# Performance work log

Hardware: AMD Instinct MI355X
Metric: run time of the kernel (lower is better)

Reference implementation:

```python
import jax, jax.numpy as jnp
import numpy as np

B, S, D, EXP = 2, 2048, 128, 16
N = D * EXP  # state_dim = 2048


def setup_inputs() -> dict:
    key = jax.random.key(0)
    ks = jax.random.split(key, 11)
    s_in = 1.0 / np.sqrt(D)   # torch Linear default init bound for dim->N layers
    s_out = 1.0 / np.sqrt(N)  # for out_proj (N->dim)
    x = jax.random.normal(ks[0], (B, S, D), dtype=jnp.float32)
    W_B = jax.random.uniform(ks[1], (N, D), jnp.float32, -s_in, s_in)
    b_B = jax.random.uniform(ks[2], (N,), jnp.float32, -s_in, s_in)
    W_C = jax.random.uniform(ks[3], (N, D), jnp.float32, -s_in, s_in)
    b_C = jax.random.uniform(ks[4], (N,), jnp.float32, -s_in, s_in)
    W_dt = jax.random.uniform(ks[5], (N, D), jnp.float32, -s_in, s_in)
    b_dt = jax.random.uniform(ks[6], (N,), jnp.float32, -s_in, s_in)
    A_log = jnp.log(jax.random.uniform(ks[7], (N,), jnp.float32) * 0.5 + 0.5)
    W_out = jax.random.uniform(ks[8], (D, N), jnp.float32, -s_out, s_out)
    b_out = jax.random.uniform(ks[9], (D,), jnp.float32, -s_out, s_out)
    return {"x": x, "W_B": W_B, "b_B": b_B, "W_C": W_C, "b_C": b_C,
            "W_dt": W_dt, "b_dt": b_dt, "A_log": A_log,
            "W_out": W_out, "b_out": b_out}


def reference(x, W_B, b_B, W_C, b_C, W_dt, b_dt, A_log, W_out, b_out):
    # Featurizer projections: [B,S,D] -> [B,S,N]
    B_feat = jnp.einsum('bsd,nd->bsn', x, W_B) + b_B
    C_feat = jnp.einsum('bsd,nd->bsn', x, W_C) + b_C
    dt = jax.nn.softplus(jnp.einsum('bsd,nd->bsn', x, W_dt) + b_dt)
    A = -jnp.exp(A_log)                # [N]
    A_bar = jnp.exp(dt * A)            # [B,S,N]
    B_bar = dt * B_feat                # [B,S,N]

    # Sequential diagonal scan: h_t = A_t * h_{t-1} + B_t ; y_t = C_t * h_t
    def step(h, abc):
        a_t, b_t, c_t = abc            # each [B,N]
        h = a_t * h + b_t
        return h, c_t * h

    h0 = jnp.zeros((x.shape[0], N), dtype=x.dtype)
    xs = (jnp.swapaxes(A_bar, 0, 1),   # [S,B,N]
          jnp.swapaxes(B_bar, 0, 1),
          jnp.swapaxes(C_feat, 0, 1))
    _, ys = jax.lax.scan(step, h0, xs)  # ys: [S,B,N]
    y = jnp.swapaxes(ys, 0, 1)          # [B,S,N]
    return jnp.einsum('bsn,dn->bsd', y, W_out) + b_out
```

## Files before the change

kernel.cpp:

```cpp
#include <hip/hip_runtime.h>


#define BB 2
#define SS 2048
#define DDIM 128
#define NDIM 2048
#define TT (BB*SS)
#define NTILE (TT/16)
#define TPB 128

typedef short short8 __attribute__((ext_vector_type(8)));
typedef float floatx4 __attribute__((ext_vector_type(4)));

__device__ __forceinline__ unsigned short f2b(float f){
  unsigned u = __float_as_uint(f);
  u += 0x7FFFu + ((u >> 16) & 1u);
  return (unsigned short)(u >> 16);
}
__device__ __forceinline__ float softplus_f(float v){
  return v > 15.f ? v : __logf(1.f + __expf(v));
}
__device__ __forceinline__ void pack8(const float* __restrict__ s,
                                      unsigned short* __restrict__ d){
  floatx4 v0 = *(const floatx4*)s;
  floatx4 v1 = *(const floatx4*)(s + 4);
  short8 r;
  r[0]=(short)f2b(v0[0]); r[1]=(short)f2b(v0[1]); r[2]=(short)f2b(v0[2]); r[3]=(short)f2b(v0[3]);
  r[4]=(short)f2b(v1[0]); r[5]=(short)f2b(v1[1]); r[6]=(short)f2b(v1[2]); r[7]=(short)f2b(v1[3]);
  *(short8*)d = r;
}

__global__ void prep_kernel(const float* __restrict__ x,
                            const float* __restrict__ W_B,
                            const float* __restrict__ W_C,
                            const float* __restrict__ W_dt,
                            const float* __restrict__ A_log,
                            const float* __restrict__ W_out,
                            unsigned short* __restrict__ xp,
                            unsigned short* __restrict__ Wp3,
                            unsigned short* __restrict__ Wop,
                            float* __restrict__ Aval){
  const int gid = blockIdx.x * blockDim.x + threadIdx.x;
  if (gid < 2048) Aval[gid] = -__expf(A_log[gid]);
  if (gid < 65536){
    int g = gid, tile = g >> 8, kk = (g >> 6) & 3, lane = g & 63;
    int q = lane >> 4, m = lane & 15;
    pack8(x + (size_t)(tile*16 + m)*DDIM + kk*32 + q*8, xp + (size_t)g*8);
  }
  if (gid < 98304){
    int mat = gid >> 15, g = gid & 32767;
    const float* W = (mat == 0) ? W_B : (mat == 1 ? W_dt : W_C);
    int tile = g >> 8, kk = (g >> 6) & 3, lane = g & 63;
    int q = lane >> 4, m = lane & 15;
    pack8(W + (size_t)(tile*16 + m)*DDIM + kk*32 + q*8,
          Wp3 + (size_t)mat*262144 + (size_t)g*8);
  }
  if (gid < 32768){
    int g = gid, tile = g >> 12, kk = (g >> 6) & 63, lane = g & 63;
    int q = lane >> 4, m = lane & 15;
    pack8(W_out + (size_t)(tile*16 + m)*NDIM + kk*32 + q*8, Wop + (size_t)g*8);
  }
}

__global__ void projscan1_kernel(const unsigned short* __restrict__ xp,
                                 const unsigned short* __restrict__ Wp3,
                                 const float* __restrict__ b_B,
                                 const float* __restrict__ b_dt,
                                 const float* __restrict__ Aval,
                                 float2* __restrict__ PH){
  __shared__ unsigned short sW[2*8192];
  const int tid  = threadIdx.x;
  const int lane = tid & 63;
  const int wv   = tid >> 6;
  const int m    = lane & 15;
  const int q    = lane >> 4;

#pragma unroll
  for (int mat = 0; mat < 2; ++mat){
    const unsigned short* src = Wp3 + (size_t)mat*262144 + (size_t)blockIdx.y*8192;
    unsigned short* dst = sW + mat*8192;
#pragma unroll
    for (int i = 0; i < 4; ++i){
      int e = (i*256 + tid) * 8;
      *(short8*)(dst + e) = *(const short8*)(src + e);
    }
  }
  __syncthreads();

  const int tileT = blockIdx.x*4 + wv;
  short8 xf[4];
#pragma unroll
  for (int kk = 0; kk < 4; ++kk)
    xf[kk] = *(const short8*)(xp + (size_t)tileT*2048 + kk*512 + lane*8);

  floatx4 acc[2][4];
#pragma unroll
  for (int mat = 0; mat < 2; ++mat)
#pragma unroll
    for (int nt = 0; nt < 4; ++nt)
      acc[mat][nt] = (floatx4){0.f,0.f,0.f,0.f};
#pragma unroll
  for (int nt = 0; nt < 4; ++nt)
#pragma unroll
    for (int kk = 0; kk < 4; ++kk){
      short8 wB = *(const short8*)(sW +          nt*2048 + kk*512 + lane*8);
      short8 wD = *(const short8*)(sW + 8192 +   nt*2048 + kk*512 + lane*8);
      acc[0][nt] = __builtin_amdgcn_mfma_f32_16x16x32_bf16(xf[kk], wB, acc[0][nt], 0, 0, 0);
      acc[1][nt] = __builtin_amdgcn_mfma_f32_16x16x32_bf16(xf[kk], wD, acc[1][nt], 0, 0, 0);
    }

  const int n0 = blockIdx.y*64;
#pragma unroll
  for (int nt = 0; nt < 4; ++nt){
    const int n = n0 + nt*16 + m;
    const float bB = b_B[n], bD = b_dt[n], Av = Aval[n];
    float Ar[4], Br[4];
#pragma unroll
    for (int r = 0; r < 4; ++r){
      float dtv = softplus_f(acc[1][nt][r] + bD);
      Ar[r] = __expf(dtv * Av);
      Br[r] = dtv * (acc[0][nt][r] + bB);
    }
    float P = Ar[0], H = Br[0];
#pragma unroll
    for (int r = 1; r < 4; ++r){ H = Ar[r]*H + Br[r]; P *= Ar[r]; }
    float pp = __shfl(P, (lane - 16) & 63, 64);
    float hh = __shfl(H, (lane - 16) & 63, 64);
    if (q >= 1){ H = P*hh + H; P = P*pp; }
    pp = __shfl(P, (lane - 32) & 63, 64);
    hh = __shfl(H, (lane - 32) & 63, 64);
    if (q >= 2){ H = P*hh + H; P = P*pp; }
    if (q == 3){
      float2 ph; ph.x = P; ph.y = H;
      PH[(size_t)tileT*NDIM + n] = ph;
    }
  }
}

__global__ void carry_kernel(const float2* __restrict__ PH,
                             float* __restrict__ initb){
  __shared__ float sP[8][32], sH[8][32], eP[8][32], eH[8][32];
  const int tid = threadIdx.x;
  const int c = tid & 31;
  const int s = tid >> 5;
  const int b = blockIdx.x >> 6;
  const int n = (blockIdx.x & 63)*32 + c;

  float Pj[16], Hj[16];
  size_t base = ((size_t)(b*TPB + s*16))*NDIM + n;
#pragma unroll
  for (int j = 0; j < 16; ++j){
    float2 ph = PH[base + (size_t)j*NDIM];
    Pj[j] = ph.x; Hj[j] = ph.y;
  }
  float P = Pj[0], H = Hj[0];
#pragma unroll
  for (int j = 1; j < 16; ++j){ H = Pj[j]*H + Hj[j]; P *= Pj[j]; }
  sP[s][c] = P; sH[s][c] = H;
  __syncthreads();
  if (tid < 32){
    float p = 1.f, h = 0.f;
#pragma unroll
    for (int ss = 0; ss < 8; ++ss){
      eP[ss][tid] = p; eH[ss][tid] = h;
      h = sP[ss][tid]*h + sH[ss][tid];
      p = sP[ss][tid]*p;
    }
  }
  __syncthreads();
  float h = eH[s][c];
#pragma unroll
  for (int j = 0; j < 16; ++j){
    initb[base + (size_t)j*NDIM] = h;
    h = Pj[j]*h + Hj[j];
  }
}

__global__ void projscan2_kernel(const unsigned short* __restrict__ xp,
                                 const unsigned short* __restrict__ Wp3,
                                 const float* __restrict__ b_B,
                                 const float* __restrict__ b_dt,
                                 const float* __restrict__ b_C,
                                 const float* __restrict__ Aval,
                                 const float* __restrict__ initb,
                                 unsigned short* __restrict__ ybp){
  __shared__ unsigned short sW[3*8192];
  __shared__ unsigned short sYT[4][16*40];
  const int tid  = threadIdx.x;
  const int lane = tid & 63;
  const int wv   = tid >> 6;
  const int m    = lane & 15;
  const int q    = lane >> 4;

#pragma unroll
  for (int mat = 0; mat < 3; ++mat){
    const unsigned short* src = Wp3 + (size_t)mat*262144 + (size_t)blockIdx.y*8192;
    unsigned short* dst = sW + mat*8192;
#pragma unroll
    for (int i = 0; i < 4; ++i){
      int e = (i*256 + tid) * 8;
      *(short8*)(dst + e) = *(const short8*)(src + e);
    }
  }
  __syncthreads();

  const int tileT = blockIdx.x*4 + wv;
  short8 xf[4];
#pragma unroll
  for (int kk = 0; kk < 4; ++kk)
    xf[kk] = *(const short8*)(xp + (size_t)tileT*2048 + kk*512 + lane*8);

  floatx4 acc[3][4];
#pragma unroll
  for (int mat = 0; mat < 3; ++mat)
#pragma unroll
    for (int nt = 0; nt < 4; ++nt)
      acc[mat][nt] = (floatx4){0.f,0.f,0.f,0.f};
#pragma unroll
  for (int nt = 0; nt < 4; ++nt)
#pragma unroll
    for (int kk = 0; kk < 4; ++kk){
      short8 wB = *(const short8*)(sW +           nt*2048 + kk*512 + lane*8);
      short8 wD = *(const short8*)(sW + 8192 +    nt*2048 + kk*512 + lane*8);
      short8 wC = *(const short8*)(sW + 16384 +   nt*2048 + kk*512 + lane*8);
      acc[0][nt] = __builtin_amdgcn_mfma_f32_16x16x32_bf16(xf[kk], wB, acc[0][nt], 0, 0, 0);
      acc[1][nt] = __builtin_amdgcn_mfma_f32_16x16x32_bf16(xf[kk], wD, acc[1][nt], 0, 0, 0);
      acc[2][nt] = __builtin_amdgcn_mfma_f32_16x16x32_bf16(xf[kk], wC, acc[2][nt], 0, 0, 0);
    }

  const int n0 = blockIdx.y*64;
  unsigned short ybuf[16];
#pragma unroll
  for (int nt = 0; nt < 4; ++nt){
    const int n = n0 + nt*16 + m;
    const float bB = b_B[n], bD = b_dt[n], bC = b_C[n], Av = Aval[n];
    const float iv = initb[(size_t)tileT*NDIM + n];
    float Ar[4], Br[4], Cc[4];
#pragma unroll
    for (int r = 0; r < 4; ++r){
      float dtv = softplus_f(acc[1][nt][r] + bD);
      Ar[r] = __expf(dtv * Av);
      Br[r] = dtv * (acc[0][nt][r] + bB);
      Cc[r] = acc[2][nt][r] + bC;
    }
    float P = Ar[0], H = Br[0];
#pragma unroll
    for (int r = 1; r < 4; ++r){ H = Ar[r]*H + Br[r]; P *= Ar[r]; }
    float pp = __shfl(P, (lane - 16) & 63, 64);
    float hh = __shfl(H, (lane - 16) & 63, 64);
    if (q >= 1){ H = P*hh + H; P = P*pp; }
    pp = __shfl(P, (lane - 32) & 63, 64);
    hh = __shfl(H, (lane - 32) & 63, 64);
    if (q >= 2){ H = P*hh + H; P = P*pp; }
    float pe = __shfl(P, (lane - 16) & 63, 64);
    float he = __shfl(H, (lane - 16) & 63, 64);
    if (q == 0){ pe = 1.f; he = 0.f; }
    float h = pe*iv + he;
#pragma unroll
    for (int r = 0; r < 4; ++r){
      h = Ar[r]*h + Br[r];
      ybuf[nt*4 + r] = f2b(Cc[r]*h);
    }
  }
#pragma unroll
  for (int p = 0; p < 2; ++p){
#pragma unroll
    for (int nt2 = 0; nt2 < 2; ++nt2){
      const int nt = 2*p + nt2;
#pragma unroll
      for (int r = 0; r < 4; ++r)
        sYT[wv][(q*4 + r)*40 + nt2*16 + m] = ybuf[nt*4 + r];
    }
    short8 af = *(const short8*)&sYT[wv][m*40 + q*8];
    const int kchunk = blockIdx.y*2 + p;
    *(short8*)(ybp + (size_t)tileT*32768 + (size_t)kchunk*512 + lane*8) = af;
  }
}

__global__ void outproj_kernel(const unsigned short* __restrict__ ybp,
                               const unsigned short* __restrict__ Wop,
                               const float* __restrict__ b_out,
                               float* __restrict__ out){
  __shared__ float red[4*2048];
  const int tid  = threadIdx.x;
  const int lane = tid & 63;
  const int wv   = tid >> 6;
  const int m    = lane & 15;
  const int q    = lane >> 4;
  const int tile = blockIdx.x;

  floatx4 acc[8];
#pragma unroll
  for (int dt = 0; dt < 8; ++dt) acc[dt] = (floatx4){0.f,0.f,0.f,0.f};

  const unsigned short* aP = ybp + (size_t)tile*32768 + lane*8;
  const unsigned short* bP = Wop + (size_t)lane*8;
#pragma unroll 4
  for (int kk = wv*16; kk < wv*16 + 16; ++kk){
    short8 af = *(const short8*)(aP + (size_t)kk*512);
#pragma unroll
    for (int dt = 0; dt < 8; ++dt){
      short8 bf = *(const short8*)(bP + (size_t)dt*32768 + (size_t)kk*512);
      acc[dt] = __builtin_amdgcn_mfma_f32_16x16x32_bf16(af, bf, acc[dt], 0, 0, 0);
    }
  }
#pragma unroll
  for (int dt = 0; dt < 8; ++dt)
#pragma unroll
    for (int r = 0; r < 4; ++r)
      red[wv*2048 + (q*4 + r)*128 + dt*16 + m] = acc[dt][r];
  __syncthreads();
#pragma unroll
  for (int i = 0; i < 8; ++i){
    int idx = i*256 + tid;
    float s = red[idx] + red[2048 + idx] + red[4096 + idx] + red[6144 + idx];
    int tl = idx >> 7, d = idx & 127;
    out[(size_t)(tile*16 + tl)*DDIM + d] = s + b_out[d];
  }
}

extern "C" void kernel_launch(void* const* d_in, const int* in_sizes, int n_in,
                              void* d_out, int out_size, void* d_ws, size_t ws_size,
                              hipStream_t stream) {
  const float* x     = (const float*)d_in[0];
  const float* W_B   = (const float*)d_in[1];
  const float* b_B   = (const float*)d_in[2];
  const float* W_C   = (const float*)d_in[3];
  const float* b_C   = (const float*)d_in[4];
  const float* W_dt  = (const float*)d_in[5];
  const float* b_dt  = (const float*)d_in[6];
  const float* A_log = (const float*)d_in[7];
  const float* W_out = (const float*)d_in[8];
  const float* b_out = (const float*)d_in[9];
  float* out = (float*)d_out;

  char* w = (char*)d_ws;
  unsigned short* xp    = (unsigned short*)(w + 0x0000000);
  unsigned short* Wp3   = (unsigned short*)(w + 0x0100000);
  unsigned short* Wop   = (unsigned short*)(w + 0x0280000);
  float*          Aval  = (float*)         (w + 0x0300000);
  float2*         PH    = (float2*)        (w + 0x0310000);
  float*          initb = (float*)         (w + 0x0710000);
  unsigned short* ybp   = (unsigned short*)(w + 0x0910000);

  prep_kernel<<<384, 256, 0, stream>>>(
      x, W_B, W_C, W_dt, A_log, W_out, xp, Wp3, Wop, Aval);

  projscan1_kernel<<<dim3(TT/64, NDIM/64), 256, 0, stream>>>(
      xp, Wp3, b_B, b_dt, Aval, PH);

  carry_kernel<<<128, 256, 0, stream>>>(PH, initb);

  projscan2_kernel<<<dim3(TT/64, NDIM/64), 256, 0, stream>>>(
      xp, Wp3, b_B, b_dt, b_C, Aval, initb, ybp);

  outproj_kernel<<<NTILE, 256, 0, stream>>>(ybp, Wop, b_out, out);
}
```

Before: 127.4 us.

## Merge two projection-scan passes into one with carry correction in outproj

Result: slower. 132.6 us (+4.1%).

```diff
diff --git a/kernel.cpp b/kernel.cpp
--- a/kernel.cpp
+++ b/kernel.cpp
@@ -16,6 +16,9 @@
   unsigned u = __float_as_uint(f);
   u += 0x7FFFu + ((u >> 16) & 1u);
   return (unsigned short)(u >> 16);
+}
+__device__ __forceinline__ float b2f(unsigned short h){
+  return __uint_as_float(((unsigned)h) << 16);
 }
 __device__ __forceinline__ float softplus_f(float v){
   return v > 15.f ? v : __logf(1.f + __expf(v));
@@ -30,23 +33,16 @@
   *(short8*)d = r;
 }
 
-__global__ void prep_kernel(const float* __restrict__ x,
-                            const float* __restrict__ W_B,
+__global__ void prep_kernel(const float* __restrict__ W_B,
                             const float* __restrict__ W_C,
                             const float* __restrict__ W_dt,
                             const float* __restrict__ A_log,
                             const float* __restrict__ W_out,
-                            unsigned short* __restrict__ xp,
                             unsigned short* __restrict__ Wp3,
                             unsigned short* __restrict__ Wop,
                             float* __restrict__ Aval){
   const int gid = blockIdx.x * blockDim.x + threadIdx.x;
   if (gid < 2048) Aval[gid] = -__expf(A_log[gid]);
-  if (gid < 65536){
-    int g = gid, tile = g >> 8, kk = (g >> 6) & 3, lane = g & 63;
-    int q = lane >> 4, m = lane & 15;
-    pack8(x + (size_t)(tile*16 + m)*DDIM + kk*32 + q*8, xp + (size_t)g*8);
-  }
   if (gid < 98304){
     int mat = gid >> 15, g = gid & 32767;
     const float* W = (mat == 0) ? W_B : (mat == 1 ? W_dt : W_C);
@@ -62,84 +58,119 @@
   }
 }
 
-__global__ void projscan1_kernel(const unsigned short* __restrict__ xp,
-                                 const unsigned short* __restrict__ Wp3,
-                                 const float* __restrict__ b_B,
-                                 const float* __restrict__ b_dt,
-                                 const float* __restrict__ Aval,
-                                 float2* __restrict__ PH){
-  __shared__ unsigned short sW[2*8192];
+__global__ void projscan_kernel(const float* __restrict__ xG,
+                                const unsigned short* __restrict__ Wp3,
+                                const float* __restrict__ b_B,
+                                const float* __restrict__ b_dt,
+                                const float* __restrict__ b_C,
+                                const float* __restrict__ Aval,
+                                unsigned short* __restrict__ ybp,
+                                unsigned short* __restrict__ coefp,
+                                float2* __restrict__ PH){
+  __shared__ unsigned short sW[3*4096];
+  __shared__ unsigned short sYT[4][16*40];
+  __shared__ unsigned short sCT[4][16*40];
   const int tid  = threadIdx.x;
   const int lane = tid & 63;
   const int wv   = tid >> 6;
   const int m    = lane & 15;
   const int q    = lane >> 4;
 
-#pragma unroll
-  for (int mat = 0; mat < 2; ++mat){
-    const unsigned short* src = Wp3 + (size_t)mat*262144 + (size_t)blockIdx.y*8192;
-    unsigned short* dst = sW + mat*8192;
-#pragma unroll
-    for (int i = 0; i < 4; ++i){
-      int e = (i*256 + tid) * 8;
-      *(short8*)(dst + e) = *(const short8*)(src + e);
-    }
+  for (int i = tid; i < 1536; i += 256){
+    int mat = i >> 9, rem = i & 511;
+    *(short8*)(sW + mat*4096 + rem*8) =
+        *(const short8*)(Wp3 + (size_t)mat*262144 + (size_t)blockIdx.y*4096 + rem*8);
   }
   __syncthreads();
 
   const int tileT = blockIdx.x*4 + wv;
   short8 xf[4];
-#pragma unroll
-  for (int kk = 0; kk < 4; ++kk)
-    xf[kk] = *(const short8*)(xp + (size_t)tileT*2048 + kk*512 + lane*8);
-
-  floatx4 acc[2][4];
-#pragma unroll
-  for (int mat = 0; mat < 2; ++mat)
-#pragma unroll
-    for (int nt = 0; nt < 4; ++nt)
+  const float* xr = xG + (size_t)(tileT*16 + m)*DDIM + q*8;
+#pragma unroll
+  for (int kk = 0; kk < 4; ++kk){
+    floatx4 u = *(const floatx4*)(xr + kk*32);
+    floatx4 v = *(const floatx4*)(xr + kk*32 + 4);
+    short8 t;
+    t[0]=(short)f2b(u[0]); t[1]=(short)f2b(u[1]); t[2]=(short)f2b(u[2]); t[3]=(short)f2b(u[3]);
+    t[4]=(short)f2b(v[0]); t[5]=(short)f2b(v[1]); t[6]=(short)f2b(v[2]); t[7]=(short)f2b(v[3]);
+    xf[kk] = t;
+  }
+
+  floatx4 acc[3][2];
+#pragma unroll
+  for (int mat = 0; mat < 3; ++mat)
+#pragma unroll
+    for (int nt = 0; nt < 2; ++nt)
       acc[mat][nt] = (floatx4){0.f,0.f,0.f,0.f};
 #pragma unroll
-  for (int nt = 0; nt < 4; ++nt)
+  for (int nt = 0; nt < 2; ++nt)
 #pragma unroll
     for (int kk = 0; kk < 4; ++kk){
-      short8 wB = *(const short8*)(sW +          nt*2048 + kk*512 + lane*8);
-      short8 wD = *(const short8*)(sW + 8192 +   nt*2048 + kk*512 + lane*8);
+      short8 wB = *(const short8*)(sW +         nt*2048 + kk*512 + lane*8);
+      short8 wD = *(const short8*)(sW + 4096 +  nt*2048 + kk*512 + lane*8);
+      short8 wC = *(const short8*)(sW + 8192 +  nt*2048 + kk*512 + lane*8);
       acc[0][nt] = __builtin_amdgcn_mfma_f32_16x16x32_bf16(xf[kk], wB, acc[0][nt], 0, 0, 0);
       acc[1][nt] = __builtin_amdgcn_mfma_f32_16x16x32_bf16(xf[kk], wD, acc[1][nt], 0, 0, 0);
-    }
-
-  const int n0 = blockIdx.y*64;
-#pragma unroll
-  for (int nt = 0; nt < 4; ++nt){
+      acc[2][nt] = __builtin_amdgcn_mfma_f32_16x16x32_bf16(xf[kk], wC, acc[2][nt], 0, 0, 0);
+    }
+
+  const int n0 = blockIdx.y*32;
+  unsigned short ybuf[8], cbuf[8];
+#pragma unroll
+  for (int nt = 0; nt < 2; ++nt){
     const int n = n0 + nt*16 + m;
-    const float bB = b_B[n], bD = b_dt[n], Av = Aval[n];
-    float Ar[4], Br[4];
+    const float bB = b_B[n], bD = b_dt[n], bC = b_C[n], Av = Aval[n];
+    float Ar[4], Br[4], Cc[4];
 #pragma unroll
     for (int r = 0; r < 4; ++r){
       float dtv = softplus_f(acc[1][nt][r] + bD);
       Ar[r] = __expf(dtv * Av);
       Br[r] = dtv * (acc[0][nt][r] + bB);
+      Cc[r] = acc[2][nt][r] + bC;
     }
     float P = Ar[0], H = Br[0];
 #pragma unroll
     for (int r = 1; r < 4; ++r){ H = Ar[r]*H + Br[r]; P *= Ar[r]; }
     float pp = __shfl(P, (lane - 16) & 63, 64);
     float hh = __shfl(H, (lane - 16) & 63, 64);
-    if (q >= 1){ H = P*hh + H; P = P*pp; }
+    if (q >= 1){ H = P*hh + H; P *= pp; }
     pp = __shfl(P, (lane - 32) & 63, 64);
     hh = __shfl(H, (lane - 32) & 63, 64);
-    if (q >= 2){ H = P*hh + H; P = P*pp; }
+    if (q >= 2){ H = P*hh + H; P *= pp; }
+    float pe = __shfl(P, (lane - 16) & 63, 64);
+    float he = __shfl(H, (lane - 16) & 63, 64);
+    if (q == 0){ pe = 1.f; he = 0.f; }
+    float h = he, pa = pe;
+#pragma unroll
+    for (int r = 0; r < 4; ++r){
+      h = Ar[r]*h + Br[r];
+      pa *= Ar[r];
+      ybuf[nt*4 + r] = f2b(Cc[r]*h);
+      cbuf[nt*4 + r] = f2b(Cc[r]*pa);
+    }
     if (q == 3){
       float2 ph; ph.x = P; ph.y = H;
       PH[(size_t)tileT*NDIM + n] = ph;
     }
   }
+
+#pragma unroll
+  for (int nt = 0; nt < 2; ++nt)
+#pragma unroll
+    for (int r = 0; r < 4; ++r){
+      sYT[wv][(q*4 + r)*40 + nt*16 + m] = ybuf[nt*4 + r];
+      sCT[wv][(q*4 + r)*40 + nt*16 + m] = cbuf[nt*4 + r];
+    }
+  short8 yv = *(const short8*)&sYT[wv][m*40 + q*8];
+  short8 cv = *(const short8*)&sCT[wv][m*40 + q*8];
+  size_t o = (size_t)tileT*32768 + (size_t)blockIdx.y*512 + (size_t)lane*8;
+  *(short8*)(ybp   + o) = yv;
+  *(short8*)(coefp + o) = cv;
 }
 
 __global__ void carry_kernel(const float2* __restrict__ PH,
                              float* __restrict__ initb){
-  __shared__ float sP[8][32], sH[8][32], eP[8][32], eH[8][32];
+  __shared__ float sP[8][32], sH[8][32], eH[8][32];
   const int tid = threadIdx.x;
   const int c = tid & 31;
   const int s = tid >> 5;
@@ -162,7 +193,7 @@
     float p = 1.f, h = 0.f;
 #pragma unroll
     for (int ss = 0; ss < 8; ++ss){
-      eP[ss][tid] = p; eH[ss][tid] = h;
+      eH[ss][tid] = h;
       h = sP[ss][tid]*h + sH[ss][tid];
       p = sP[ss][tid]*p;
     }
@@ -176,108 +207,9 @@
   }
 }
 
-__global__ void projscan2_kernel(const unsigned short* __restrict__ xp,
-                                 const unsigned short* __restrict__ Wp3,
-                                 const float* __restrict__ b_B,
-                                 const float* __restrict__ b_dt,
-                                 const float* __restrict__ b_C,
-                                 const float* __restrict__ Aval,
-                                 const float* __restrict__ initb,
-                                 unsigned short* __restrict__ ybp){
-  __shared__ unsigned short sW[3*8192];
-  __shared__ unsigned short sYT[4][16*40];
-  const int tid  = threadIdx.x;
-  const int lane = tid & 63;
-  const int wv   = tid >> 6;
-  const int m    = lane & 15;
-  const int q    = lane >> 4;
-
-#pragma unroll
-  for (int mat = 0; mat < 3; ++mat){
-    const unsigned short* src = Wp3 + (size_t)mat*262144 + (size_t)blockIdx.y*8192;
-    unsigned short* dst = sW + mat*8192;
-#pragma unroll
-    for (int i = 0; i < 4; ++i){
-      int e = (i*256 + tid) * 8;
-      *(short8*)(dst + e) = *(const short8*)(src + e);
-    }
-  }
-  __syncthreads();
-
-  const int tileT = blockIdx.x*4 + wv;
-  short8 xf[4];
-#pragma unroll
-  for (int kk = 0; kk < 4; ++kk)
-    xf[kk] = *(const short8*)(xp + (size_t)tileT*2048 + kk*512 + lane*8);
-
-  floatx4 acc[3][4];
-#pragma unroll
-  for (int mat = 0; mat < 3; ++mat)
-#pragma unroll
-    for (int nt = 0; nt < 4; ++nt)
-      acc[mat][nt] = (floatx4){0.f,0.f,0.f,0.f};
-#pragma unroll
-  for (int nt = 0; nt < 4; ++nt)
-#pragma unroll
-    for (int kk = 0; kk < 4; ++kk){
-      short8 wB = *(const short8*)(sW +           nt*2048 + kk*512 + lane*8);
-      short8 wD = *(const short8*)(sW + 8192 +    nt*2048 + kk*512 + lane*8);
-      short8 wC = *(const short8*)(sW + 16384 +   nt*2048 + kk*512 + lane*8);
-      acc[0][nt] = __builtin_amdgcn_mfma_f32_16x16x32_bf16(xf[kk], wB, acc[0][nt], 0, 0, 0);
-      acc[1][nt] = __builtin_amdgcn_mfma_f32_16x16x32_bf16(xf[kk], wD, acc[1][nt], 0, 0, 0);
-      acc[2][nt] = __builtin_amdgcn_mfma_f32_16x16x32_bf16(xf[kk], wC, acc[2][nt], 0, 0, 0);
-    }
-
-  const int n0 = blockIdx.y*64;
-  unsigned short ybuf[16];
-#pragma unroll
-  for (int nt = 0; nt < 4; ++nt){
-    const int n = n0 + nt*16 + m;
-    const float bB = b_B[n], bD = b_dt[n], bC = b_C[n], Av = Aval[n];
-    const float iv = initb[(size_t)tileT*NDIM + n];
-    float Ar[4], Br[4], Cc[4];
-#pragma unroll
-    for (int r = 0; r < 4; ++r){
-      float dtv = softplus_f(acc[1][nt][r] + bD);
-      Ar[r] = __expf(dtv * Av);
-      Br[r] = dtv * (acc[0][nt][r] + bB);
-      Cc[r] = acc[2][nt][r] + bC;
-    }
-    float P = Ar[0], H = Br[0];
-#pragma unroll
-    for (int r = 1; r < 4; ++r){ H = Ar[r]*H + Br[r]; P *= Ar[r]; }
-    float pp = __shfl(P, (lane - 16) & 63, 64);
-    float hh = __shfl(H, (lane - 16) & 63, 64);
-    if (q >= 1){ H = P*hh + H; P = P*pp; }
-    pp = __shfl(P, (lane - 32) & 63, 64);
-    hh = __shfl(H, (lane - 32) & 63, 64);
-    if (q >= 2){ H = P*hh + H; P = P*pp; }
-    float pe = __shfl(P, (lane - 16) & 63, 64);
-    float he = __shfl(H, (lane - 16) & 63, 64);
-    if (q == 0){ pe = 1.f; he = 0.f; }
-    float h = pe*iv + he;
-#pragma unroll
-    for (int r = 0; r < 4; ++r){
-      h = Ar[r]*h + Br[r];
-      ybuf[nt*4 + r] = f2b(Cc[r]*h);
-    }
-  }
-#pragma unroll
-  for (int p = 0; p < 2; ++p){
-#pragma unroll
-    for (int nt2 = 0; nt2 < 2; ++nt2){
-      const int nt = 2*p + nt2;
-#pragma unroll
-      for (int r = 0; r < 4; ++r)
-        sYT[wv][(q*4 + r)*40 + nt2*16 + m] = ybuf[nt*4 + r];
-    }
-    short8 af = *(const short8*)&sYT[wv][m*40 + q*8];
-    const int kchunk = blockIdx.y*2 + p;
-    *(short8*)(ybp + (size_t)tileT*32768 + (size_t)kchunk*512 + lane*8) = af;
-  }
-}
-
 __global__ void outproj_kernel(const unsigned short* __restrict__ ybp,
+                               const unsigned short* __restrict__ coefp,
+                               const float* __restrict__ initb,
                                const unsigned short* __restrict__ Wop,
                                const float* __restrict__ b_out,
                                float* __restrict__ out){
@@ -293,11 +225,23 @@
 #pragma unroll
   for (int dt = 0; dt < 8; ++dt) acc[dt] = (floatx4){0.f,0.f,0.f,0.f};
 
-  const unsigned short* aP = ybp + (size_t)tile*32768 + lane*8;
+  const unsigned short* aP = ybp   + (size_t)tile*32768 + lane*8;
+  const unsigned short* cP = coefp + (size_t)tile*32768 + lane*8;
+  const float*          iB = initb + (size_t)tile*NDIM + q*8;
   const unsigned short* bP = Wop + (size_t)lane*8;
 #pragma unroll 4
   for (int kk = wv*16; kk < wv*16 + 16; ++kk){
-    short8 af = *(const short8*)(aP + (size_t)kk*512);
+    short8 yl = *(const short8*)(aP + (size_t)kk*512);
+    short8 cf = *(const short8*)(cP + (size_t)kk*512);
+    floatx4 i0 = *(const floatx4*)(iB + kk*32);
+    floatx4 i1 = *(const floatx4*)(iB + kk*32 + 4);
+    short8 af;
+#pragma unroll
+    for (int j = 0; j < 4; ++j)
+      af[j] = (short)f2b(b2f((unsigned short)yl[j]) + b2f((unsigned short)cf[j])*i0[j]);
+#pragma unroll
+    for (int j = 0; j < 4; ++j)
+      af[4+j] = (short)f2b(b2f((unsigned short)yl[4+j]) + b2f((unsigned short)cf[4+j])*i1[j]);
 #pragma unroll
     for (int dt = 0; dt < 8; ++dt){
       short8 bf = *(const short8*)(bP + (size_t)dt*32768 + (size_t)kk*512);
@@ -335,24 +279,22 @@
   float* out = (float*)d_out;
 
   char* w = (char*)d_ws;
-  unsigned short* xp    = (unsigned short*)(w + 0x0000000);
-  unsigned short* Wp3   = (unsigned short*)(w + 0x0100000);
-  unsigned short* Wop   = (unsigned short*)(w + 0x0280000);
-  float*          Aval  = (float*)         (w + 0x0300000);
-  float2*         PH    = (float2*)        (w + 0x0310000);
-  float*          initb = (float*)         (w + 0x0710000);
-  unsigned short* ybp   = (unsigned short*)(w + 0x0910000);
+  unsigned short* Wp3   = (unsigned short*)(w + 0x0000000);
+  unsigned short* Wop   = (unsigned short*)(w + 0x0180000);
+  float*          Aval  = (float*)         (w + 0x0200000);
+  float2*         PH    = (float2*)        (w + 0x0210000);
+  float*          initb = (float*)         (w + 0x0610000);
+  unsigned short* ybp   = (unsigned short*)(w + 0x0810000);
+  unsigned short* coefp = (unsigned short*)(w + 0x1810000);
 
   prep_kernel<<<384, 256, 0, stream>>>(
-      x, W_B, W_C, W_dt, A_log, W_out, xp, Wp3, Wop, Aval);
-
-  projscan1_kernel<<<dim3(TT/64, NDIM/64), 256, 0, stream>>>(
-      xp, Wp3, b_B, b_dt, Aval, PH);
+      W_B, W_C, W_dt, A_log, W_out, Wp3, Wop, Aval);
+
+  projscan_kernel<<<dim3(TT/64, NDIM/32), 256, 0, stream>>>(
+      x, Wp3, b_B, b_dt, b_C, Aval, ybp, coefp, PH);
 
   carry_kernel<<<128, 256, 0, stream>>>(PH, initb);
 
-  projscan2_kernel<<<dim3(TT/64, NDIM/64), 256, 0, stream>>>(
-      xp, Wp3, b_B, b_dt, b_C, Aval, initb, ybp);
-
-  outproj_kernel<<<NTILE, 256, 0, stream>>>(ybp, Wop, b_out, out);
-}
+  outproj_kernel<<<NTILE, 256, 0, stream>>>(
+      ybp, coefp, initb, Wop, b_out, out);
+}
```
